# Kernel tuning notes

Hardware: AMD Instinct MI355X
Metric: run time of the kernel (lower is better)

## Reference

```python
import jax, jax.numpy as jnp
import numpy as np

B, N, H, NH, M = 4, 8192, 1024, 16, 64
D = H // NH  # head_dim = 64
SCALE = D ** -0.5


def setup_inputs() -> dict:
    key = jax.random.key(0)
    ks = jax.random.split(key, 10)
    inp = {
        'x': jax.random.normal(ks[0], (B, N, H), jnp.float32),
        'c': jax.random.normal(ks[1], (B, H), jnp.float32),
        'w_kv': jax.random.normal(ks[2], (H, 2 * H), jnp.float32) * (H ** -0.5),
        'b_kv': jnp.zeros((2 * H,), jnp.float32),
        'w_temp': jax.random.normal(ks[3], (H, NH), jnp.float32) * (H ** -0.5),
        'b_temp': jnp.zeros((NH,), jnp.float32),
        'xq': jax.random.normal(ks[4], (NH, M, D), jnp.float32) * (D ** -0.5),
        'qkv_proj': jax.random.normal(ks[5], (NH, D, 3 * D), jnp.float32) * 0.02,
        'w_out': jax.random.normal(ks[6], (H, H), jnp.float32) * (H ** -0.5),
        'b_out': jnp.zeros((H,), jnp.float32),
    }
    return inp


def reference(x, c, w_kv, b_kv, w_temp, b_temp, xq, qkv_proj, w_out, b_out):
    b, n, h = x.shape
    # kv slice projections -> [b, h, n, d]
    kv = x @ w_kv + b_kv
    xk, xv = jnp.split(kv, 2, axis=-1)
    xk = xk.reshape(b, n, NH, D).transpose(0, 2, 1, 3)
    xv = xv.reshape(b, n, NH, D).transpose(0, 2, 1, 3)
    # per-token learned temperature: [b, n, heads] -> [b, heads, 1, n]
    temperature = 0.5 + jax.nn.softplus(x @ w_temp + b_temp)
    temperature = temperature.transpose(0, 2, 1)[:, :, None, :]
    # slice scores and softmax over SLICE (query) dim m
    slice_scores = jnp.einsum('hmd,bhnd->bhmn', xq, xk)
    slice_weights = jax.nn.softmax(slice_scores / temperature, axis=-2)
    slice_norm = slice_weights.sum(axis=-1)  # [b, h, m]
    slice_token = jnp.einsum('bhmn,bhnd->bhmd', slice_weights, xv)
    slice_token = slice_token / (slice_norm[..., None] + 1e-5)
    # tiny intra-slice 'attention' (faithfully elementwise, softmax over d)
    qkv = jnp.einsum('bhmd,hde->bhme', slice_token, qkv_proj)
    q_t, k_t, v_t = jnp.split(qkv, 3, axis=-1)
    dots = q_t * k_t * SCALE          # einsum 'bhqd,bhdq->bhqd' == elementwise
    attn = jax.nn.softmax(dots, axis=-1)
    out_slice_token = attn * v_t       # einsum 'bhqd,bhqd->bhqd' == elementwise
    # scatter back to tokens via slice_weights
    out_x = jnp.einsum('bhmd,bhmn->bhnd', out_slice_token, slice_weights)
    out_x = out_x.transpose(0, 2, 1, 3).reshape(b, n, h)
    return out_x @ w_out + b_out
```

## Files before the change

kernel.cpp:

```cpp
#include <hip/hip_runtime.h>
#include <hip/hip_bf16.h>


#define NTOK 32768
#define HH   1024
#define NHD  16
#define DD   64

typedef short short8 __attribute__((ext_vector_type(8)));
typedef float f32x4 __attribute__((ext_vector_type(4)));

#define AS1 __attribute__((address_space(1)))
#define AS3 __attribute__((address_space(3)))

__device__ __forceinline__ void glds16(const void* g, void* l) {
  __builtin_amdgcn_global_load_lds((const AS1 void*)g, (AS3 void*)l, 16, 0, 0);
}

__device__ __forceinline__ void split1(float v, __hip_bfloat16& h, __hip_bfloat16& l) {
  h = __float2bfloat16(v);
  l = __float2bfloat16(v - __bfloat162float(h));
}


__global__ __launch_bounds__(256) void k_acat_t(const float* __restrict__ w_kv,
                                                const float* __restrict__ xq,
                                                __hip_bfloat16* __restrict__ wbth,
                                                __hip_bfloat16* __restrict__ wbtl) {
  int hd = blockIdx.x >> 3, kt = blockIdx.x & 7, k0 = kt * 128;
  __shared__ float xqs[64 * 65];
  __shared__ float wks[128 * 65];
  int t = threadIdx.x;
  for (int j = 0; j < 16; ++j) {
    int idx = t + 256 * j; int m = idx >> 6, d = idx & 63;
    xqs[m * 65 + d] = xq[hd * 4096 + idx];
  }
  for (int j = 0; j < 32; ++j) {
    int idx = t + 256 * j; int r = idx >> 6, c = idx & 63;
    wks[r * 65 + c] = w_kv[(size_t)(k0 + r) * 2048 + hd * 64 + c];
  }
  __syncthreads();
  int m = t & 63, kg = t >> 6;
  __hip_bfloat16 hbuf[32], lbuf[32];
  for (int i = 0; i < 32; ++i) {
    int k = kg * 32 + i;
    float s = 0.f;
    #pragma unroll 8
    for (int d = 0; d < 64; ++d) s = fmaf(wks[k * 65 + d], xqs[m * 65 + d], s);
    split1(s, hbuf[i], lbuf[i]);
  }
  size_t o = (size_t)(hd * 64 + m) * 1024 + k0 + kg * 32;
  for (int i = 0; i < 32; i += 8) {
    *(uint4*)&wbth[o + i] = *(uint4*)&hbuf[i];
    *(uint4*)&wbtl[o + i] = *(uint4*)&lbuf[i];
  }
}

__global__ __launch_bounds__(256) void k_tsplit(const float* __restrict__ src, int ld,
                                                __hip_bfloat16* __restrict__ dh,
                                                __hip_bfloat16* __restrict__ dl) {
  __shared__ float tile[64 * 65];
  int br = blockIdx.y * 64, bc = blockIdx.x * 64;
  int t = threadIdx.x;
  for (int j = 0; j < 16; ++j) {
    int idx = t + 256 * j; int r = idx >> 6, c = idx & 63;
    tile[r * 65 + c] = src[(size_t)(br + r) * ld + bc + c];
  }
  __syncthreads();
  for (int j = 0; j < 16; ++j) {
    int idx = t + 256 * j; int c = idx >> 6, r = idx & 63;
    float v = tile[r * 65 + c];
    __hip_bfloat16 hv, lv; split1(v, hv, lv);
    size_t o = (size_t)(bc + c) * 1024 + br + r;
    dh[o] = hv; dl[o] = lv;
  }
}

__global__ void k_split(const float* __restrict__ src, __hip_bfloat16* __restrict__ hi,
                        __hip_bfloat16* __restrict__ lo) {
  size_t base = ((size_t)blockIdx.x * 256 + threadIdx.x) * 8;
  float4 v0 = *(const float4*)&src[base];
  float4 v1 = *(const float4*)&src[base + 4];
  float vv[8] = {v0.x, v0.y, v0.z, v0.w, v1.x, v1.y, v1.z, v1.w};
  __hip_bfloat16 h8[8], l8[8];
  #pragma unroll
  for (int i = 0; i < 8; ++i) split1(vv[i], h8[i], l8[i]);
  *(uint4*)&hi[base] = *(uint4*)h8;
  *(uint4*)&lo[base] = *(uint4*)l8;
}

__global__ __launch_bounds__(512, 2) void k_mfma8(
    const __hip_bfloat16* __restrict__ Ah, const __hip_bfloat16* __restrict__ Al,
    const __hip_bfloat16* __restrict__ Bh, const __hip_bfloat16* __restrict__ Bl,
    const float* __restrict__ bias, float* __restrict__ C, int ldc) {
  __shared__ __align__(16) char lds[131072];
  const int t = threadIdx.x;
  const int w = t >> 6, lane = t & 63;

  const int gx = gridDim.x;
  const int nwg = gx * gridDim.y;
  const int bid = blockIdx.y * gx + blockIdx.x;
  const int swzb = (bid & 7) * (nwg >> 3) + (bid >> 3);
  const int n0 = (swzb % gx) * 256;
  const int m0 = (swzb / gx) * 256;

  const int wr = w >> 2, wc = w & 3;
  const int fm = lane & 15, kq = lane >> 4;

  int offA[8], offB[4];
  #pragma unroll
  for (int i = 0; i < 8; ++i) {
    int row = wr * 128 + i * 16 + fm;
    offA[i] = (row >> 1) * 128 + ((((row & 1) << 2) | kq) ^ ((row >> 1) & 7)) * 16;
  }
  #pragma unroll
  for (int j = 0; j < 4; ++j) {
    int row = wc * 64 + j * 16 + fm;
    offB[j] = (row >> 1) * 128 + ((((row & 1) << 2) | kq) ^ ((row >> 1) & 7)) * 16;
  }

  const int sp = lane >> 3, su = (lane & 7) ^ sp;
  const int srow = 2 * sp + (su >> 2);
  const int scol = (su & 3) * 8;
  const int aO0 = (m0 + w * 16 + srow) * 1024 + scol;
  const int aO1 = aO0 + 128 * 1024;
  const int bO0 = (n0 + w * 16 + srow) * 1024 + scol;
  const int bO1 = bO0 + 128 * 1024;
  const int ldst = w * 1024 + lane * 16;

  f32x4 acc[8][4];
  #pragma unroll
  for (int i = 0; i < 8; ++i)
    #pragma unroll
    for (int j = 0; j < 4; ++j) acc[i][j] = (f32x4){0.f, 0.f, 0.f, 0.f};

  auto stageA = [&](int ts) {
    int seg = ts >> 5, koff = (ts & 31) * 32;
    const __hip_bfloat16* src = (seg == 1) ? Al : Ah;
    char* dst = &lds[(ts & 3) * 32768];
    glds16(src + aO0 + koff, dst + ldst);
    glds16(src + aO1 + koff, dst + 8192 + ldst);
  };
  auto stageB = [&](int ts) {
    int seg = ts >> 5, koff = (ts & 31) * 32;
    const __hip_bfloat16* src = (seg == 2) ? Bl : Bh;
    char* dst = &lds[(ts & 3) * 32768 + 16384];
    glds16(src + bO0 + koff, dst + ldst);
    glds16(src + bO1 + koff, dst + 8192 + ldst);
  };

  stageA(0); stageB(0);
  stageA(1); stageB(1);
  stageA(2); stageB(2);
  asm volatile("s_waitcnt vmcnt(8)" ::: "memory");
  __builtin_amdgcn_s_barrier();
  __builtin_amdgcn_sched_barrier(0);

  short8 bfr[4];
  #pragma unroll 4
  for (int tt = 0; tt < 96; ++tt) {
    const char* ab = &lds[(tt & 3) * 32768];
    const char* bb = ab + 16384;
    int ts = tt + 3; if (ts > 95) ts = 95;

    #pragma unroll
    for (int j = 0; j < 4; ++j) bfr[j] = *(const short8*)(bb + offB[j]);
    short8 afr[4];
    #pragma unroll
    for (int i = 0; i < 4; ++i) afr[i] = *(const short8*)(ab + offA[i]);
    stageA(ts);
    __builtin_amdgcn_s_barrier();
    __builtin_amdgcn_sched_barrier(0);
    __builtin_amdgcn_s_setprio(1);
    #pragma unroll
    for (int i = 0; i < 4; ++i)
      #pragma unroll
      for (int j = 0; j < 4; ++j)
        acc[i][j] = __builtin_amdgcn_mfma_f32_16x16x32_bf16(afr[i], bfr[j], acc[i][j], 0, 0, 0);
    __builtin_amdgcn_s_setprio(0);
    __builtin_amdgcn_s_barrier();
    __builtin_amdgcn_sched_barrier(0);

    #pragma unroll
    for (int i = 0; i < 4; ++i) afr[i] = *(const short8*)(ab + offA[4 + i]);
    stageB(ts);
    __builtin_amdgcn_s_barrier();
    __builtin_amdgcn_sched_barrier(0);
    __builtin_amdgcn_s_setprio(1);
    #pragma unroll
    for (int i = 0; i < 4; ++i)
      #pragma unroll
      for (int j = 0; j < 4; ++j)
        acc[4 + i][j] = __builtin_amdgcn_mfma_f32_16x16x32_bf16(afr[i], bfr[j], acc[4 + i][j], 0, 0, 0);
    __builtin_amdgcn_s_setprio(0);
    asm volatile("s_waitcnt vmcnt(8)" ::: "memory");
    __builtin_amdgcn_s_barrier();
    __builtin_amdgcn_sched_barrier(0);
  }

  asm volatile("s_waitcnt vmcnt(0)" ::: "memory");
  __builtin_amdgcn_s_barrier();
  __builtin_amdgcn_sched_barrier(0);

  const int cm = (lane >> 4) * 4, cn = lane & 15;
  #pragma unroll
  for (int j = 0; j < 4; ++j) {
    int col = n0 + wc * 64 + j * 16 + cn;
    float bbv = bias[col];
    #pragma unroll
    for (int i = 0; i < 8; ++i) {
      int row = m0 + wr * 128 + i * 16 + cm;
      f32x4 v = acc[i][j];
      #pragma unroll
      for (int r = 0; r < 4; ++r)
        C[(size_t)(row + r) * ldc + col] = v[r] + bbv;
    }
  }
}

__global__ __launch_bounds__(256) void k_acat(const float* __restrict__ w_kv,
                                              const float* __restrict__ xq,
                                              float* __restrict__ wbig) {
  int h = blockIdx.x >> 3, kt = blockIdx.x & 7, k0 = kt * 128;
  __shared__ float xqs[64 * 68];
  __shared__ float wks[128 * 68];
  int t = threadIdx.x;
  for (int j = 0; j < 16; ++j) {
    int idx = t + 256 * j; int m = idx >> 6, d = idx & 63;
    xqs[m * 68 + d] = xq[h * 4096 + idx];
  }
  for (int j = 0; j < 32; ++j) {
    int idx = t + 256 * j; int r = idx >> 6, c = idx & 63;
    wks[r * 68 + c] = w_kv[(k0 + r) * 2048 + h * 64 + c];
  }
  __syncthreads();
  int k = t >> 1, half = t & 1;
  float out[32];
  for (int mi = 0; mi < 32; ++mi) {
    int m = half * 32 + mi;
    float s = 0.f;
    #pragma unroll 8
    for (int d = 0; d < 64; ++d) s = fmaf(wks[k * 68 + d], xqs[m * 68 + d], s);
    out[mi] = s;
  }
  float* dst = &wbig[(k0 + k) * 2048 + h * 64 + half * 32];
  for (int mi = 0; mi < 32; mi += 4)
    *(float4*)(dst + mi) = make_float4(out[mi], out[mi + 1], out[mi + 2], out[mi + 3]);
}

__global__ void k_copyv(const float* __restrict__ w_kv, float* __restrict__ wbig) {
  int idx4 = blockIdx.x * 256 + threadIdx.x;
  int k = idx4 >> 8, j4 = idx4 & 255;
  int off = k * 2048 + 1024 + j4 * 4;
  *(float4*)(wbig + off) = *(const float4*)(w_kv + off);
}

__global__ void k_bias1(const float* __restrict__ xq, const float* __restrict__ b_kv,
                        float* __restrict__ bias1) {
  int j = blockIdx.x * 256 + threadIdx.x;
  if (j < 1024) {
    int h = j >> 6, m = j & 63;
    float s = 0.f;
    for (int d = 0; d < 64; ++d) s = fmaf(xq[h * 4096 + m * 64 + d], b_kv[h * 64 + d], s);
    bias1[j] = s;
  } else {
    bias1[j] = b_kv[j];
  }
}

__global__ __launch_bounds__(256) void k_temp(const float* __restrict__ x,
                                              const float* __restrict__ w_temp,
                                              const float* __restrict__ b_temp,
                                              float* __restrict__ T) {
  __shared__ float xs[16 * 1028];
  int t = threadIdx.x;
  int bn0 = blockIdx.x * 16;
  for (int j = 0; j < 16; ++j) {
    int idx4 = t + 256 * j; int row = idx4 >> 8, c4 = (idx4 & 255) * 4;
    *(float4*)&xs[row * 1028 + c4] = *(const float4*)&x[(bn0 + row) * 1024 + c4];
  }
  __syncthreads();
  int tok = t >> 4, j = t & 15;
  float z = b_temp[j];
  for (int k = 0; k < 1024; ++k) z = fmaf(xs[tok * 1028 + k], w_temp[k * 16 + j], z);
  float sp = fmaxf(z, 0.f) + log1pf(expf(-fabsf(z)));
  T[(bn0 + tok) * 16 + j] = 0.5f + sp;
}

__global__ __launch_bounds__(256) void k_gemm(const float* __restrict__ A, int lda,
                                              const float* __restrict__ Bm, int ldb,
                                              const float* __restrict__ bias,
                                              float* __restrict__ C, int ldc, int K) {
  __shared__ float As[8 * 132];
  __shared__ float Bs[8 * 132];
  int t = threadIdx.x;
  int m0 = blockIdx.y * 128, n0 = blockIdx.x * 128;
  int ar = t >> 1, ac = (t & 1) * 4;
  int bk = t >> 5, bc = (t & 31) * 4;
  const float* Ag = A + (size_t)(m0 + ar) * lda + ac;
  const float* Bg = Bm + (size_t)bk * ldb + n0 + bc;
  int tx = t & 15, ty = t >> 4;
  float acc[8][8] = {};
  float4 a4 = *(const float4*)Ag;
  float4 b4 = *(const float4*)Bg;
  for (int kt = 0; kt < K; kt += 8) {
    __syncthreads();
    As[(ac + 0) * 132 + ar] = a4.x;
    As[(ac + 1) * 132 + ar] = a4.y;
    As[(ac + 2) * 132 + ar] = a4.z;
    As[(ac + 3) * 132 + ar] = a4.w;
    *(float4*)&Bs[bk * 132 + bc] = b4;
    __syncthreads();
    if (kt + 8 < K) {
      a4 = *(const float4*)(Ag + kt + 8);
      b4 = *(const float4*)(Bg + (size_t)(kt + 8) * ldb);
    }
    #pragma unroll
    for (int k = 0; k < 8; ++k) {
      float av[8], bv[8];
      *(float4*)&av[0] = *(float4*)&As[k * 132 + ty * 8];
      *(float4*)&av[4] = *(float4*)&As[k * 132 + ty * 8 + 4];
      *(float4*)&bv[0] = *(float4*)&Bs[k * 132 + tx * 4];
      *(float4*)&bv[4] = *(float4*)&Bs[k * 132 + 64 + tx * 4];
      #pragma unroll
      for (int i = 0; i < 8; ++i)
        #pragma unroll
        for (int j = 0; j < 8; ++j) acc[i][j] = fmaf(av[i], bv[j], acc[i][j]);
    }
  }
  float4 bb0 = *(const float4*)&bias[n0 + tx * 4];
  float4 bb1 = *(const float4*)&bias[n0 + 64 + tx * 4];
  #pragma unroll
  for (int i = 0; i < 8; ++i) {
    float* crow = C + (size_t)(m0 + ty * 8 + i) * ldc + n0;
    float4 o0 = make_float4(acc[i][0] + bb0.x, acc[i][1] + bb0.y,
                            acc[i][2] + bb0.z, acc[i][3] + bb0.w);
    float4 o1 = make_float4(acc[i][4] + bb1.x, acc[i][5] + bb1.y,
                            acc[i][6] + bb1.z, acc[i][7] + bb1.w);
    *(float4*)&crow[tx * 4] = o0;
    *(float4*)&crow[64 + tx * 4] = o1;
  }
}

__global__ __launch_bounds__(256) void k_smax(float* __restrict__ S, const float* __restrict__ T,
                                              float* __restrict__ token, float* __restrict__ norm) {
  int pair = blockIdx.x >> 3, chunk = blockIdx.x & 7;
  int b = pair >> 4, h = pair & 15;
  __shared__ float sm[128 * 68];
  __shared__ float xv[128 * 68];
  int t = threadIdx.x;
  int m = t >> 2, dg = t & 3;
  float acc[16] = {};
  float nacc = 0.f;
  for (int s = 0; s < 8; ++s) {
    int bn0 = b * 8192 + chunk * 1024 + s * 128;
    for (int jj = 0; jj < 8; ++jj) {
      int idx4 = t + 256 * jj; int row = idx4 >> 4, c4 = (idx4 & 15) * 4;
      int g = (bn0 + row) * 2048 + h * 64 + c4;
      *(float4*)&sm[row * 68 + c4] = *(const float4*)&S[g];
      *(float4*)&xv[row * 68 + c4] = *(const float4*)&S[g + 1024];
    }
    __syncthreads();
    if (t < 128) {
      float tt = T[(bn0 + t) * 16 + h];
      float inv = 1.f / tt;
      float* row = &sm[t * 68];
      float mx = -1e30f;
      for (int mm = 0; mm < 64; ++mm) mx = fmaxf(mx, row[mm]);
      float sum = 0.f;
      for (int mm = 0; mm < 64; ++mm) { float e = expf((row[mm] - mx) * inv); row[mm] = e; sum += e; }
      float sinv = 1.f / sum;
      for (int mm = 0; mm < 64; ++mm) row[mm] *= sinv;
    }
    __syncthreads();
    for (int jj = 0; jj < 8; ++jj) {
      int idx4 = t + 256 * jj; int row = idx4 >> 4, c4 = (idx4 & 15) * 4;
      int g = (bn0 + row) * 2048 + h * 64 + c4;
      *(float4*)&S[g] = *(const float4*)&sm[row * 68 + c4];
    }
    for (int n = 0; n < 128; ++n) {
      float w = sm[n * 68 + m];
      if (dg == 0) nacc += w;
      const float* xr = &xv[n * 68 + dg * 16];
      #pragma unroll
      for (int q = 0; q < 4; ++q) {
        float4 v = *(const float4*)&xr[q * 4];
        acc[q * 4 + 0] = fmaf(w, v.x, acc[q * 4 + 0]);
        acc[q * 4 + 1] = fmaf(w, v.y, acc[q * 4 + 1]);
        acc[q * 4 + 2] = fmaf(w, v.z, acc[q * 4 + 2]);
        acc[q * 4 + 3] = fmaf(w, v.w, acc[q * 4 + 3]);
      }
    }
    __syncthreads();
  }
  int tb = pair * 4096 + m * 64 + dg * 16;
  for (int q = 0; q < 16; ++q) atomicAdd(&token[tb + q], acc[q]);
  if (dg == 0) atomicAdd(&norm[pair * 64 + m], nacc);
}

__global__ __launch_bounds__(256) void k_stagec(const float* __restrict__ token,
                                                const float* __restrict__ norm,
                                                const float* __restrict__ proj,
                                                float* __restrict__ ost) {
  int pair = blockIdx.x; int h = pair & 15;
  __shared__ float st[64 * 68];
  __shared__ float qk[64 * 196];
  int t = threadIdx.x;
  for (int j = 0; j < 16; ++j) {
    int idx = t + 256 * j; int m = idx >> 6, d = idx & 63;
    st[m * 68 + d] = token[pair * 4096 + idx] / (norm[pair * 64 + m] + 1e-5f);
  }
  __syncthreads();
  for (int idx = t; idx < 64 * 192; idx += 256) {
    int m = idx / 192, e = idx % 192;
    float s = 0.f;
    const float* pr = &proj[h * 12288 + e];
    const float* sr = &st[m * 68];
    for (int d = 0; d < 64; ++d) s = fmaf(sr[d], pr[d * 192], s);
    qk[m * 196 + e] = s;
  }
  __syncthreads();
  if (t < 64) {
    const float* q = &qk[t * 196];
    float dots[64];
    float mx = -1e30f;
    for (int d = 0; d < 64; ++d) { dots[d] = q[d] * q[64 + d] * 0.125f; mx = fmaxf(mx, dots[d]); }
    float sum = 0.f;
    for (int d = 0; d < 64; ++d) { dots[d] = expf(dots[d] - mx); sum += dots[d]; }
    float sinv = 1.f / sum;
    for (int d = 0; d < 64; ++d) ost[pair * 4096 + t * 64 + d] = dots[d] * sinv * q[128 + d];
  }
}

__global__ __launch_bounds__(256) void k_staged(float* __restrict__ S, const float* __restrict__ ost) {
  int pair = blockIdx.x >> 6, chunk = blockIdx.x & 63;
  int b = pair >> 4, h = pair & 15;
  __shared__ float ws[128 * 68];
  int t = threadIdx.x;
  int bn0 = b * 8192 + chunk * 128;
  for (int jj = 0; jj < 8; ++jj) {
    int idx4 = t + 256 * jj; int row = idx4 >> 4, c4 = (idx4 & 15) * 4;
    *(float4*)&ws[row * 68 + c4] = *(const float4*)&S[(bn0 + row) * 2048 + h * 64 + c4];
  }
  int d = t & 63, ng = t >> 6;
  float o[64];
  #pragma unroll
  for (int mm = 0; mm < 64; ++mm) o[mm] = ost[pair * 4096 + mm * 64 + d];
  __syncthreads();
  for (int i = 0; i < 32; ++i) {
    int n = ng + 4 * i;
    const float* wr = &ws[n * 68];
    float s = 0.f;
    #pragma unroll
    for (int mm = 0; mm < 64; ++mm) s = fmaf(wr[mm], o[mm], s);
    S[(bn0 + n) * 2048 + 1024 + h * 64 + d] = s;
  }
}

__global__ __launch_bounds__(256) void k_staged_bf(const float* __restrict__ S,
                                                   const float* __restrict__ ost,
                                                   __hip_bfloat16* __restrict__ oxh,
                                                   __hip_bfloat16* __restrict__ oxl) {
  int pair = blockIdx.x >> 6, chunk = blockIdx.x & 63;
  int b = pair >> 4, hd = pair & 15;
  __shared__ float ws[128 * 68];
  int t = threadIdx.x;
  int bn0 = b * 8192 + chunk * 128;
  for (int jj = 0; jj < 8; ++jj) {
    int idx4 = t + 256 * jj; int row = idx4 >> 4, c4 = (idx4 & 15) * 4;
    *(float4*)&ws[row * 68 + c4] = *(const float4*)&S[(bn0 + row) * 2048 + hd * 64 + c4];
  }
  int d = t & 63, ng = t >> 6;
  float o[64];
  #pragma unroll
  for (int mm = 0; mm < 64; ++mm) o[mm] = ost[pair * 4096 + mm * 64 + d];
  __syncthreads();
  for (int i = 0; i < 32; ++i) {
    int n = ng + 4 * i;
    const float* wr = &ws[n * 68];
    float s = 0.f;
    #pragma unroll
    for (int mm = 0; mm < 64; ++mm) s = fmaf(wr[mm], o[mm], s);
    __hip_bfloat16 hv, lv; split1(s, hv, lv);
    size_t oo = (size_t)(bn0 + n) * 1024 + hd * 64 + d;
    oxh[oo] = hv; oxl[oo] = lv;
  }
}

extern "C" void kernel_launch(void* const* d_in, const int* in_sizes, int n_in,
                              void* d_out, int out_size, void* d_ws, size_t ws_size,
                              hipStream_t stream) {
  const float* x      = (const float*)d_in[0];
  const float* w_kv   = (const float*)d_in[2];
  const float* b_kv   = (const float*)d_in[3];
  const float* w_temp = (const float*)d_in[4];
  const float* b_temp = (const float*)d_in[5];
  const float* xq     = (const float*)d_in[6];
  const float* proj   = (const float*)d_in[7];
  const float* w_out  = (const float*)d_in[8];
  const float* b_out  = (const float*)d_in[9];
  float* out = (float*)d_out;

  float* ws    = (float*)d_ws;
  float* S     = ws;
  float* T     = S + 67108864;
  float* BIAS1 = T + 524288;
  float* TOKEN = BIAS1 + 2048;
  float* NORM  = TOKEN + 262144;
  float* OST   = NORM + 4096;
  float* FEND  = OST + 262144;
  __hip_bfloat16* WbTh = (__hip_bfloat16*)FEND;
  __hip_bfloat16* WbTl = WbTh + 2097152;
  __hip_bfloat16* WoTh = WbTl + 2097152;
  __hip_bfloat16* WoTl = WoTh + 1048576;
  __hip_bfloat16* XH   = WoTl + 1048576;
  __hip_bfloat16* XL   = XH + 33554432;
  const size_t need_fast = 419454976ULL;

  hipMemsetAsync(TOKEN, 0, (262144 + 4096) * sizeof(float), stream);
  k_bias1<<<8, 256, 0, stream>>>(xq, b_kv, BIAS1);
  k_temp<<<2048, 256, 0, stream>>>(x, w_temp, b_temp, T);

  if (ws_size >= need_fast) {
    k_acat_t<<<128, 256, 0, stream>>>(w_kv, xq, WbTh, WbTl);
    k_tsplit<<<dim3(16, 16), 256, 0, stream>>>(w_kv + 1024, 2048,
                                               WbTh + 1048576, WbTl + 1048576);
    k_tsplit<<<dim3(16, 16), 256, 0, stream>>>(w_out, 1024, WoTh, WoTl);
    k_split<<<16384, 256, 0, stream>>>(x, XH, XL);
    k_mfma8<<<dim3(8, 128), 512, 0, stream>>>(XH, XL, WbTh, WbTl, BIAS1, S, 2048);
    k_smax<<<512, 256, 0, stream>>>(S, T, TOKEN, NORM);
    k_stagec<<<64, 256, 0, stream>>>(TOKEN, NORM, proj, OST);
    k_staged_bf<<<4096, 256, 0, stream>>>(S, OST, XH, XL);
    k_mfma8<<<dim3(4, 128), 512, 0, stream>>>(XH, XL, WoTh, WoTl, b_out, out, 1024);
  } else {
    float* WBIG = (float*)WbTh;
    k_acat<<<128, 256, 0, stream>>>(w_kv, xq, WBIG);
    k_copyv<<<1024, 256, 0, stream>>>(w_kv, WBIG);
    k_gemm<<<dim3(16, 256), 256, 0, stream>>>(x, 1024, WBIG, 2048, BIAS1, S, 2048, 1024);
    k_smax<<<512, 256, 0, stream>>>(S, T, TOKEN, NORM);
    k_stagec<<<64, 256, 0, stream>>>(TOKEN, NORM, proj, OST);
    k_staged<<<4096, 256, 0, stream>>>(S, OST);
    k_gemm<<<dim3(8, 256), 256, 0, stream>>>(S + 1024, 2048, w_out, 1024, b_out, out, 1024, 1024);
  }
}
```

Baseline: 1.457 ms.

## Load hi/lo split operands together per k-step and reuse fragments across products

The split-bf16 GEMM used to walk three concatenated K segments (hi*hi, lo*hi, hi*lo) as 96 separate tiles in a 4-deep LDS ring. It now stages Ah, Al, Bh and Bl for one k-slice together into a double-buffered 64KB region and runs 32 iterations. Each iteration computes all three products, reusing the Ah and Bh fragments across them, which cuts LDS fragment reads. In exchange the prefetch depth drops from three tiles ahead to one, with a full vmcnt(0) wait every iteration, so global-load latency may be less well hidden. Register pressure also rises from holding 8 A fragments plus two sets of B fragments.

```diff
diff --git a/kernel.cpp b/kernel.cpp
--- a/kernel.cpp
+++ b/kernel.cpp
@@ -134,73 +134,77 @@
     #pragma unroll
     for (int j = 0; j < 4; ++j) acc[i][j] = (f32x4){0.f, 0.f, 0.f, 0.f};
 
-  auto stageA = [&](int ts) {
-    int seg = ts >> 5, koff = (ts & 31) * 32;
-    const __hip_bfloat16* src = (seg == 1) ? Al : Ah;
-    char* dst = &lds[(ts & 3) * 32768];
-    glds16(src + aO0 + koff, dst + ldst);
-    glds16(src + aO1 + koff, dst + 8192 + ldst);
+  auto stage = [&](int ts, char* buf) {
+    int koff = ts * 32;
+    glds16(Ah + aO0 + koff, buf + ldst);
+    glds16(Ah + aO1 + koff, buf + 8192 + ldst);
+    glds16(Al + aO0 + koff, buf + 16384 + ldst);
+    glds16(Al + aO1 + koff, buf + 24576 + ldst);
+    glds16(Bh + bO0 + koff, buf + 32768 + ldst);
+    glds16(Bh + bO1 + koff, buf + 40960 + ldst);
+    glds16(Bl + bO0 + koff, buf + 49152 + ldst);
+    glds16(Bl + bO1 + koff, buf + 57344 + ldst);
   };
-  auto stageB = [&](int ts) {
-    int seg = ts >> 5, koff = (ts & 31) * 32;
-    const __hip_bfloat16* src = (seg == 2) ? Bl : Bh;
-    char* dst = &lds[(ts & 3) * 32768 + 16384];
-    glds16(src + bO0 + koff, dst + ldst);
-    glds16(src + bO1 + koff, dst + 8192 + ldst);
-  };
-
-  stageA(0); stageB(0);
-  stageA(1); stageB(1);
-  stageA(2); stageB(2);
-  asm volatile("s_waitcnt vmcnt(8)" ::: "memory");
+
+  stage(0, lds);
+  asm volatile("s_waitcnt vmcnt(0)" ::: "memory");
   __builtin_amdgcn_s_barrier();
   __builtin_amdgcn_sched_barrier(0);
 
-  short8 bfr[4];
-  #pragma unroll 4
-  for (int tt = 0; tt < 96; ++tt) {
-    const char* ab = &lds[(tt & 3) * 32768];
-    const char* bb = ab + 16384;
-    int ts = tt + 3; if (ts > 95) ts = 95;
-
-    #pragma unroll
-    for (int j = 0; j < 4; ++j) bfr[j] = *(const short8*)(bb + offB[j]);
-    short8 afr[4];
-    #pragma unroll
-    for (int i = 0; i < 4; ++i) afr[i] = *(const short8*)(ab + offA[i]);
-    stageA(ts);
+  #pragma unroll 2
+  for (int tt = 0; tt < 32; ++tt) {
+    char* rb = &lds[(tt & 1) * 65536];
+    char* wb = &lds[((tt + 1) & 1) * 65536];
+
+    short8 ah[8], bh[4], xb[4];
+    #pragma unroll
+    for (int i = 0; i < 8; ++i) ah[i] = *(const short8*)(rb + offA[i]);
+    #pragma unroll
+    for (int j = 0; j < 4; ++j) bh[j] = *(const short8*)(rb + 32768 + offB[j]);
+    if (tt < 31) stage(tt + 1, wb);
     __builtin_amdgcn_s_barrier();
     __builtin_amdgcn_sched_barrier(0);
     __builtin_amdgcn_s_setprio(1);
     #pragma unroll
-    for (int i = 0; i < 4; ++i)
+    for (int i = 0; i < 8; ++i)
       #pragma unroll
       for (int j = 0; j < 4; ++j)
-        acc[i][j] = __builtin_amdgcn_mfma_f32_16x16x32_bf16(afr[i], bfr[j], acc[i][j], 0, 0, 0);
+        acc[i][j] = __builtin_amdgcn_mfma_f32_16x16x32_bf16(ah[i], bh[j], acc[i][j], 0, 0, 0);
     __builtin_amdgcn_s_setprio(0);
     __builtin_amdgcn_s_barrier();
     __builtin_amdgcn_sched_barrier(0);
 
     #pragma unroll
-    for (int i = 0; i < 4; ++i) afr[i] = *(const short8*)(ab + offA[4 + i]);
-    stageB(ts);
+    for (int j = 0; j < 4; ++j) xb[j] = *(const short8*)(rb + 49152 + offB[j]);
     __builtin_amdgcn_s_barrier();
     __builtin_amdgcn_sched_barrier(0);
     __builtin_amdgcn_s_setprio(1);
     #pragma unroll
-    for (int i = 0; i < 4; ++i)
+    for (int i = 0; i < 8; ++i)
       #pragma unroll
       for (int j = 0; j < 4; ++j)
-        acc[4 + i][j] = __builtin_amdgcn_mfma_f32_16x16x32_bf16(afr[i], bfr[j], acc[4 + i][j], 0, 0, 0);
+        acc[i][j] = __builtin_amdgcn_mfma_f32_16x16x32_bf16(ah[i], xb[j], acc[i][j], 0, 0, 0);
     __builtin_amdgcn_s_setprio(0);
-    asm volatile("s_waitcnt vmcnt(8)" ::: "memory");
     __builtin_amdgcn_s_barrier();
     __builtin_amdgcn_sched_barrier(0);
+
+    #pragma unroll
+    for (int i = 0; i < 8; ++i) ah[i] = *(const short8*)(rb + 16384 + offA[i]);
+    __builtin_amdgcn_s_barrier();
+    __builtin_amdgcn_sched_barrier(0);
+    __builtin_amdgcn_s_setprio(1);
+    #pragma unroll
+    for (int i = 0; i < 8; ++i)
+      #pragma unroll
+      for (int j = 0; j < 4; ++j)
+        acc[i][j] = __builtin_amdgcn_mfma_f32_16x16x32_bf16(ah[i], bh[j], acc[i][j], 0, 0, 0);
+    __builtin_amdgcn_s_setprio(0);
+    asm volatile("s_waitcnt vmcnt(0)" ::: "memory");
+    __builtin_amdgcn_s_barrier();
+    __builtin_amdgcn_sched_barrier(0);
   }
 
   asm volatile("s_waitcnt vmcnt(0)" ::: "memory");
-  __builtin_amdgcn_s_barrier();
-  __builtin_amdgcn_sched_barrier(0);
 
   const int cm = (lane >> 4) * 4, cn = lane & 15;
   #pragma unroll
```

Result: slower. 1.534 ms (+5.3%).
